# Kernel tuning notes

Hardware: AMD Instinct MI355X
Metric: run time of the kernel (lower is better)

The kernel has to match this reference:

```python
import jax, jax.numpy as jnp
import numpy as np


def setup_inputs() -> dict:
    key = jax.random.key(0)
    ks = jax.random.split(key, 9)
    B, S, I, H, L, O = 64, 1024, 64, 256, 2, 1
    sc = 1.0 / np.sqrt(H)
    return {
        "x": jax.random.normal(ks[0], (B, S, I), dtype=jnp.float32),
        "theta": jax.random.normal(ks[1], (I, H), dtype=jnp.float32) * 0.01,
        "phi": jax.random.normal(ks[2], (I, H), dtype=jnp.float32) * 0.01,
        "W_ih": jax.random.normal(ks[3], (L, 4 * H, H), dtype=jnp.float32) * sc,
        "W_hh": jax.random.normal(ks[4], (L, 4 * H, H), dtype=jnp.float32) * sc,
        "b_ih": jax.random.normal(ks[5], (L, 4 * H), dtype=jnp.float32) * sc,
        "b_hh": jax.random.normal(ks[6], (L, 4 * H), dtype=jnp.float32) * sc,
        "W_fc": jax.random.normal(ks[7], (O, H), dtype=jnp.float32) * sc,
        "b_fc": jax.random.normal(ks[8], (O,), dtype=jnp.float32) * sc,
    }


def _quantum(x, theta, phi):
    # Per-call Gaussian noise on the phase parameters (fixed key for determinism)
    k1, k2 = jax.random.split(jax.random.key(42))
    tn = jax.random.normal(k1, theta.shape, theta.dtype) * 0.01
    pn = jax.random.normal(k2, phi.shape, phi.dtype) * 0.01
    psi_r = jnp.cos(theta + tn)  # real part of psi
    psi_i = jnp.sin(phi + pn)    # imag part of psi
    # sum over input dim of x * psi == matmul; |complex| = sqrt(re^2 + im^2)
    yr = jnp.einsum('bsi,ih->bsh', x, psi_r)
    yi = jnp.einsum('bsi,ih->bsh', x, psi_i)
    return jnp.sqrt(yr * yr + yi * yi)


def _lstm_layer(inp, Wi, Wh, bi, bh):
    # inp: (B,S,H). PyTorch gate order: i, f, g, o.
    H = Wh.shape[-1]
    B = inp.shape[0]
    pre = jnp.einsum('bsh,gh->bsg', inp, Wi) + bi + bh  # (B,S,4H)

    def step(carry, xt):
        h, c = carry
        g = xt + h @ Wh.T
        i_, f_, g_, o_ = jnp.split(g, 4, axis=-1)
        i_ = jax.nn.sigmoid(i_)
        f_ = jax.nn.sigmoid(f_)
        o_ = jax.nn.sigmoid(o_)
        g_ = jnp.tanh(g_)
        c = f_ * c + i_ * g_
        h = o_ * jnp.tanh(c)
        return (h, c), h

    h0 = jnp.zeros((B, H), inp.dtype)
    (_, _), hs = jax.lax.scan(step, (h0, h0), jnp.swapaxes(pre, 0, 1))
    return jnp.swapaxes(hs, 0, 1)  # (B,S,H)


def reference(x, theta, phi, W_ih, W_hh, b_ih, b_hh, W_fc, b_fc):
    out = _quantum(x, theta, phi)
    for l in range(W_ih.shape[0]):
        out = _lstm_layer(out, W_ih[l], W_hh[l], b_ih[l], b_hh[l])
    return out[:, -1, :] @ W_fc.T + b_fc
```

## Files before the change

### kernel.cpp

```cpp
#include <hip/hip_runtime.h>

typedef _Float16 f16;
typedef _Float16 f16x2 __attribute__((ext_vector_type(2)));
typedef _Float16 f16x8 __attribute__((ext_vector_type(8)));
typedef float f32x4 __attribute__((ext_vector_type(4)));

#define B_ 64
#define S_ 1024
#define I_ 64
#define H_ 256
#define G_ 1024
#define M_ 65536

__device__ __forceinline__ unsigned rotl32(unsigned x, int r){ return (x<<r)|(x>>(32-r)); }

__device__ __forceinline__ void threefry(unsigned k0, unsigned k1, unsigned& x0, unsigned& x1){
  unsigned k2 = k0 ^ k1 ^ 0x1BD11BDAu;
  x0 += k0; x1 += k1;
  x0 += x1; x1 = rotl32(x1,13); x1 ^= x0;
  x0 += x1; x1 = rotl32(x1,15); x1 ^= x0;
  x0 += x1; x1 = rotl32(x1,26); x1 ^= x0;
  x0 += x1; x1 = rotl32(x1, 6); x1 ^= x0;
  x0 += k1; x1 += k2 + 1u;
  x0 += x1; x1 = rotl32(x1,17); x1 ^= x0;
  x0 += x1; x1 = rotl32(x1,29); x1 ^= x0;
  x0 += x1; x1 = rotl32(x1,16); x1 ^= x0;
  x0 += x1; x1 = rotl32(x1,24); x1 ^= x0;
  x0 += k2; x1 += k0 + 2u;
  x0 += x1; x1 = rotl32(x1,13); x1 ^= x0;
  x0 += x1; x1 = rotl32(x1,15); x1 ^= x0;
  x0 += x1; x1 = rotl32(x1,26); x1 ^= x0;
  x0 += x1; x1 = rotl32(x1, 6); x1 ^= x0;
  x0 += k0; x1 += k1 + 3u;
  x0 += x1; x1 = rotl32(x1,17); x1 ^= x0;
  x0 += x1; x1 = rotl32(x1,29); x1 ^= x0;
  x0 += x1; x1 = rotl32(x1,16); x1 ^= x0;
  x0 += x1; x1 = rotl32(x1,24); x1 ^= x0;
  x0 += k1; x1 += k2 + 4u;
  x0 += x1; x1 = rotl32(x1,13); x1 ^= x0;
  x0 += x1; x1 = rotl32(x1,15); x1 ^= x0;
  x0 += x1; x1 = rotl32(x1,26); x1 ^= x0;
  x0 += x1; x1 = rotl32(x1, 6); x1 ^= x0;
  x0 += k2; x1 += k0 + 5u;
}

__device__ __forceinline__ float erfinv_f(float x){
  float w = -log1pf(-x*x);
  float p;
  if (w < 5.f){
    w -= 2.5f;
    p = 2.81022636e-08f;
    p = fmaf(p,w, 3.43273939e-07f);
    p = fmaf(p,w,-3.5233877e-06f);
    p = fmaf(p,w,-4.39150654e-06f);
    p = fmaf(p,w, 0.00021858087f);
    p = fmaf(p,w,-0.00125372503f);
    p = fmaf(p,w,-0.00417768164f);
    p = fmaf(p,w, 0.246640727f);
    p = fmaf(p,w, 1.50140941f);
  } else {
    w = sqrtf(w) - 3.f;
    p = -0.000200214257f;
    p = fmaf(p,w, 0.000100950558f);
    p = fmaf(p,w, 0.00134934322f);
    p = fmaf(p,w,-0.00367342844f);
    p = fmaf(p,w, 0.00573950773f);
    p = fmaf(p,w,-0.0076224613f);
    p = fmaf(p,w, 0.00943887047f);
    p = fmaf(p,w, 1.00167406f);
    p = fmaf(p,w, 2.83297682f);
  }
  return p*x;
}

__device__ __forceinline__ float jax_normal_from_bits(unsigned bits){
  unsigned fb = (bits >> 9) | 0x3f800000u;
  float f = __uint_as_float(fb) - 1.0f;
  const float lo = -0.9999999403953552f;
  float u = fmaf(f, 2.0f, lo);
  u = fmaxf(lo, u);
  return 1.4142135623730951f * erfinv_f(u);
}

__global__ __launch_bounds__(256) void prep_psi(const float* __restrict__ theta,
                                                const float* __restrict__ phi,
                                                unsigned* __restrict__ psiP){
  int j = blockIdx.x*256 + threadIdx.x;
  unsigned a0=0u, a1=0u; threefry(0u,42u,a0,a1);
  unsigned b0=0u, b1=1u; threefry(0u,42u,b0,b1);
  unsigned t0=0u, t1=(unsigned)j; threefry(a0,a1,t0,t1);
  unsigned p0=0u, p1=(unsigned)j; threefry(b0,b1,p0,p1);
  float tn = 0.01f * jax_normal_from_bits(t0^t1);
  float pn = 0.01f * jax_normal_from_bits(p0^p1);
  float cr = cosf(theta[j] + tn);
  float ci = sinf(phi[j]   + pn);
  f16x2 pk; pk.x = (f16)cr; pk.y = (f16)ci;
  psiP[j] = __builtin_bit_cast(unsigned, pk);
}

__global__ __launch_bounds__(256) void pack_wh(const float* __restrict__ Whh,
                                               uint4* __restrict__ WhT4){
  int idx = blockIdx.x*256 + threadIdx.x;
  int l   = idx >> 15;
  int row = (idx >> 5) & 1023;
  int kk  = idx & 31;
  const float* src = Whh + ((size_t)(l*1024 + row))*256 + kk*8;
  f16x8 tmp;
  #pragma unroll
  for (int j=0;j<8;j++) tmp[j] = (f16)src[j];
  WhT4[l*32768 + kk*1024 + row] = __builtin_bit_cast(uint4, tmp);
}

__global__ __launch_bounds__(256) void pack_wi_bias(const float* __restrict__ Wih,
                                                    const float* __restrict__ bih,
                                                    const float* __restrict__ bhh,
                                                    f16* __restrict__ WiH,
                                                    float* __restrict__ biasS){
  int idx = blockIdx.x*256 + threadIdx.x;
  WiH[idx] = (f16)Wih[idx];
  if (idx < 2048) biasS[idx] = bih[idx] + bhh[idx];
}

__global__ __launch_bounds__(128) void zero_prog(int* __restrict__ p){
  p[threadIdx.x] = 0;
}

__global__ __launch_bounds__(256) void quantum_k(const float* __restrict__ x,
                                                 const unsigned* __restrict__ psiP,
                                                 f16* __restrict__ yq){
  __shared__ float xs[64];
  int m = blockIdx.x;
  int n = threadIdx.x;
  if (n < 64) xs[n] = x[(size_t)m*64 + n];
  __syncthreads();
  float ar=0.f, ai=0.f;
  #pragma unroll 8
  for (int k=0;k<64;k++){
    unsigned p = psiP[k*256 + n];
    f16x2 pk = __builtin_bit_cast(f16x2, p);
    float xv = xs[k];
    ar = fmaf(xv, (float)pk.x, ar);
    ai = fmaf(xv, (float)pk.y, ai);
  }
  yq[(size_t)m*256 + n] = (f16)sqrtf(ar*ar + ai*ai);
}

__global__ __launch_bounds__(256,2) void pre_gemm(const f16* __restrict__ A,
                                                  const f16* __restrict__ W,
                                                  const float* __restrict__ bias,
                                                  f16* __restrict__ out){
  const int m0 = blockIdx.x*64;
  const int n0 = blockIdx.y*512;
  __shared__ f16 As[64*264];
  const int tid = threadIdx.x;
  #pragma unroll
  for (int it=0; it<8; ++it){
    int u = tid + it*256;
    int row = u >> 5, ko = u & 31;
    f16x8 v = *(const f16x8*)(A + (size_t)(m0+row)*256 + ko*8);
    *(f16x8*)(&As[row*264 + ko*8]) = v;
  }
  __syncthreads();
  const int wave = tid >> 6, lane = tid & 63;
  const int n_w = n0 + wave*128;
  const int lr = lane & 15, lk = (lane>>4)*8;
  f32x4 acc[4][8] = {};
  for (int ks=0; ks<8; ++ks){
    f16x8 a[4];
    #pragma unroll
    for (int mt=0; mt<4; ++mt)
      a[mt] = *(const f16x8*)(&As[(mt*16+lr)*264 + ks*32 + lk]);
    #pragma unroll
    for (int nt=0; nt<8; ++nt){
      f16x8 b = *(const f16x8*)(W + (size_t)(n_w + nt*16 + lr)*256 + ks*32 + lk);
      #pragma unroll
      for (int mt=0; mt<4; ++mt)
        acc[mt][nt] = __builtin_amdgcn_mfma_f32_16x16x32_f16(a[mt], b, acc[mt][nt], 0,0,0);
    }
  }
  const int col = lr, rbase = (lane>>4)*4;
  #pragma unroll
  for (int nt=0; nt<8; ++nt){
    float bv = bias[n_w + nt*16 + col];
    #pragma unroll
    for (int mt=0; mt<4; ++mt){
      #pragma unroll
      for (int j=0; j<4; ++j){
        int m = m0 + mt*16 + rbase + j;
        out[(size_t)m*1024 + n_w + nt*16 + col] = (f16)(acc[mt][nt][j] + bv);
      }
    }
  }
}

__device__ __forceinline__ float sigm_f(float x){
  x = fminf(fmaxf(x,-30.f),30.f);
  return 1.f/(1.f + __expf(-x));
}
__device__ __forceinline__ float tanh_f(float x){
  x = fminf(fmaxf(x,-15.f),15.f);
  float e = __expf(-2.f*x);
  return (1.f-e)/(1.f+e);
}
__device__ __forceinline__ float dot2f(unsigned w, unsigned h, float acc){
#if __has_builtin(__builtin_amdgcn_fdot2)
  return __builtin_amdgcn_fdot2(__builtin_bit_cast(f16x2,w), __builtin_bit_cast(f16x2,h), acc, false);
#else
  float d;
  asm("v_dot2_f32_f16 %0, %1, %2, %3" : "=v"(d) : "v"(w), "v"(h), "v"(acc));
  return d;
#endif
}

__device__ __forceinline__ f32x4 mfma16(uint4 a, uint4 b, f32x4 c){
  return __builtin_amdgcn_mfma_f32_16x16x32_f16(
      __builtin_bit_cast(f16x8, a), __builtin_bit_cast(f16x8, b), c, 0, 0, 0);
}

template<int WRITE_ALL, int CONSUME>
__device__ __forceinline__
void lstm_core(const f16* __restrict__ preB,
               const uint4* __restrict__ Wh,
               f16* __restrict__ outh,
               f16* __restrict__ hfin_p,
               int* __restrict__ prog_rel,
               int* __restrict__ prog_acq,
               uint4* wlds, uint4* h4, float* gbuf)
{
  const int tid = threadIdx.x;
  uint4 w[23];
  #pragma unroll
  for (int j=0;j<23;++j) w[j] = Wh[j*1024 + tid];
  #pragma unroll
  for (int j=0;j<5;++j)  wlds[j*1024 + tid] = Wh[(23+j)*1024 + tid];
  if (tid < 32) h4[tid] = make_uint4(0u,0u,0u,0u);
  float c = 0.f;

  if (CONSUME){
    if (tid==0){
      while (__hip_atomic_load(prog_acq, __ATOMIC_ACQUIRE, __HIP_MEMORY_SCOPE_AGENT) < 1)
        __builtin_amdgcn_s_sleep(8);
    }
  }
  __syncthreads();

  float pv = (float)preB[tid];
  const int gtype = tid >> 8;
  const uint4* wstr = Wh + 28*1024 + tid;

  for (int t=0; t<1024; ++t){
    if (CONSUME){
      if ((t&15)==15 && t<1023){
        if (tid==0){
          const int need = ((t+1)>>4) + 1;
          while (__hip_atomic_load(prog_acq, __ATOMIC_ACQUIRE, __HIP_MEMORY_SCOPE_AGENT) < need)
            __builtin_amdgcn_s_sleep(8);
        }
        __syncthreads();
      }
    }
    float pn = (t < 1023) ? (float)preB[(size_t)(t+1)*1024 + tid] : 0.f;
    uint4 s0 = wstr[0];
    uint4 s1 = wstr[1024];
    uint4 s2 = wstr[2048];
    uint4 s3 = wstr[3072];
    float a0 = pv, a1 = 0.f;

    uint4 hb0 = h4[0], hb1 = h4[1];
    uint4 ub0 = wlds[tid], ub1 = wlds[1024 + tid];

    #pragma unroll
    for (int kk=0; kk<23; ++kk){
      uint4 hp = (kk & 1) ? hb1 : hb0;
      if (kk & 1) hb1 = h4[kk+2]; else hb0 = h4[kk+2];
      a0 = dot2f(w[kk].x, hp.x, a0); a1 = dot2f(w[kk].y, hp.y, a1);
      a0 = dot2f(w[kk].z, hp.z, a0); a1 = dot2f(w[kk].w, hp.w, a1);
    }
    #pragma unroll
    for (int j=0; j<5; ++j){
      const int kk = 23 + j;
      uint4 hp = (kk & 1) ? hb1 : hb0;
      if (kk & 1) hb1 = h4[kk+2]; else hb0 = h4[kk+2];
      uint4 u = (j & 1) ? ub1 : ub0;
      if (j + 2 < 5){ if (j & 1) ub1 = wlds[(j+2)*1024 + tid]; else ub0 = wlds[(j+2)*1024 + tid]; }
      a0 = dot2f(u.x, hp.x, a0); a1 = dot2f(u.y, hp.y, a1);
      a0 = dot2f(u.z, hp.z, a0); a1 = dot2f(u.w, hp.w, a1);
    }
    #pragma unroll
    for (int j=0; j<4; ++j){
      const int kk = 28 + j;
      uint4 hp = (kk & 1) ? hb1 : hb0;
      if (kk + 2 < 32){ if (kk & 1) hb1 = h4[kk+2]; else hb0 = h4[kk+2]; }
      const uint4 u = (j==0) ? s0 : (j==1) ? s1 : (j==2) ? s2 : s3;
      a0 = dot2f(u.x, hp.x, a0); a1 = dot2f(u.y, hp.y, a1);
      a0 = dot2f(u.z, hp.z, a0); a1 = dot2f(u.w, hp.w, a1);
    }

    {
      const float raw = a0 + a1;
      gbuf[tid] = (gtype == 2) ? tanh_f(raw) : sigm_f(raw);
    }
    __syncthreads();
    if (tid < 256){
      float i_ = gbuf[tid];
      float f_ = gbuf[256+tid];
      float g_ = gbuf[512+tid];
      float o_ = gbuf[768+tid];
      c = fmaf(f_, c, i_*g_);
      float h = o_ * tanh_f(c);
      ((f16*)h4)[tid] = (f16)h;
      if (WRITE_ALL) outh[(size_t)t*256 + tid] = (f16)h;
      else if (t == 1023) hfin_p[tid] = (f16)h;
    }
    __syncthreads();
    if (WRITE_ALL){
      if ((t&15)==15 && tid==0){
        __threadfence();
        __hip_atomic_store(prog_rel, t+1, __ATOMIC_RELEASE, __HIP_MEMORY_SCOPE_AGENT);
      }
    }
    pv = pn;
  }
}

__device__ __forceinline__
void gemm_role(const f16* __restrict__ h1b,
               const f16* __restrict__ W2,
               const float* __restrict__ bias2,
               f16* __restrict__ pre2b,
               int* __restrict__ prog1b,
               int* __restrict__ prog2b)
{
  const int tid  = threadIdx.x;
  const int w    = tid >> 6, lane = tid & 63;
  const int lr   = lane & 15, lq = lane >> 4;
  for (int cidx=0; cidx<64; ++cidx){
    if (tid==0){
      while (__hip_atomic_load(prog1b, __ATOMIC_ACQUIRE, __HIP_MEMORY_SCOPE_AGENT) < 16*(cidx+1))
        __builtin_amdgcn_s_sleep(8);
    }
    __syncthreads();
    const int t0 = cidx*16;
    const f16* Ab = h1b + ((size_t)(t0 + lr))*256 + lq*8;
    uint4 af[8];
    #pragma unroll
    for (int ks=0; ks<8; ++ks) af[ks] = *(const uint4*)(Ab + ks*32);
    #pragma unroll
    for (int nt=0; nt<4; ++nt){
      f32x4 acc = {0.f,0.f,0.f,0.f};
      const int gate = w*64 + nt*16 + lr;
      const f16* Bb = W2 + (size_t)gate*256 + lq*8;
      #pragma unroll
      for (int ks=0; ks<8; ++ks){
        const uint4 bf = *(const uint4*)(Bb + ks*32);
        acc = mfma16(af[ks], bf, acc);
      }
      const float bv = bias2[gate];
      #pragma unroll
      for (int j=0; j<4; ++j){
        const int t = t0 + lq*4 + j;
        pre2b[(size_t)t*1024 + gate] = (f16)(acc[j] + bv);
      }
    }
    asm volatile("s_waitcnt vmcnt(0)" ::: "memory");
    __syncthreads();
    if (tid==0){
      __threadfence();
      __hip_atomic_store(prog2b, cidx+1, __ATOMIC_RELEASE, __HIP_MEMORY_SCOPE_AGENT);
    }
  }
}

__global__ __launch_bounds__(1024, 4)
void pipeline_k(const f16* __restrict__ pre1,
                const uint4* __restrict__ WhT4,
                const f16* __restrict__ W2,
                const float* __restrict__ biasS,
                f16* __restrict__ h1,
                f16* __restrict__ pre2,
                f16* __restrict__ hfin,
                int* __restrict__ prog1,
                int* __restrict__ prog2)
{
  __shared__ __align__(16) uint4 wlds[5*1024];
  __shared__ __align__(16) uint4 h4[32];
  __shared__ float gbuf[1024];
  const int bid = blockIdx.x;
  if (bid < 64){
    const int b = bid;
    lstm_core<1,0>(pre1 + (size_t)b*1024*1024, WhT4,
                   h1 + (size_t)b*1024*256, nullptr,
                   prog1 + b, nullptr, wlds, h4, gbuf);
  } else if (bid < 128){
    const int b = bid - 64;
    gemm_role(h1 + (size_t)b*1024*256, W2, biasS + 1024,
              pre2 + (size_t)b*1024*1024, prog1 + b, prog2 + b);
  } else {
    const int b = bid - 128;
    lstm_core<0,1>(pre2 + (size_t)b*1024*1024, WhT4 + 32768,
                   nullptr, hfin + b*256,
                   nullptr, prog2 + b, wlds, h4, gbuf);
  }
}

__global__ __launch_bounds__(64) void fc_k(const f16* __restrict__ hfin,
                                           const float* __restrict__ Wfc,
                                           const float* __restrict__ bfc,
                                           float* __restrict__ out){
  int b = blockIdx.x, k = threadIdx.x;
  float a = 0.f;
  #pragma unroll
  for (int j=0;j<4;j++){
    int idx = k + 64*j;
    a += (float)hfin[b*256 + idx] * Wfc[idx];
  }
  #pragma unroll
  for (int off=32; off; off>>=1) a += __shfl_down(a, off);
  if (k==0) out[b] = a + bfc[0];
}

extern "C" void kernel_launch(void* const* d_in, const int* in_sizes, int n_in,
                              void* d_out, int out_size, void* d_ws, size_t ws_size,
                              hipStream_t stream) {
  const float* x     = (const float*)d_in[0];
  const float* theta = (const float*)d_in[1];
  const float* phi   = (const float*)d_in[2];
  const float* Wih   = (const float*)d_in[3];
  const float* Whh   = (const float*)d_in[4];
  const float* bih   = (const float*)d_in[5];
  const float* bhh   = (const float*)d_in[6];
  const float* Wfc   = (const float*)d_in[7];
  const float* bfc   = (const float*)d_in[8];
  float* out = (float*)d_out;

  char* ws = (char*)d_ws;
  size_t off = 0;
  auto take = [&](size_t bytes){ size_t r = off; off += (bytes + 255) & ~(size_t)255; return r; };
  f16*      pre1  = (f16*)     (ws + take((size_t)M_*1024*2));
  f16*      pre2  = pre1;
  f16*      yq    = (f16*)     (ws + take((size_t)M_*256*2));
  f16*      h1    = (f16*)     (ws + take((size_t)M_*256*2));
  unsigned* psiP  = (unsigned*)(ws + take((size_t)16384*4));
  uint4*    WhT4  = (uint4*)   (ws + take((size_t)2*32768*16));
  f16*      WiH   = (f16*)     (ws + take((size_t)2*262144*2));
  float*    biasS = (float*)   (ws + take((size_t)2048*4));
  f16*      hfin  = (f16*)     (ws + take((size_t)64*256*2));
  int*      prog1 = (int*)     (ws + take((size_t)64*4));
  int*      prog2 = (int*)     (ws + take((size_t)64*4));

  zero_prog   <<<1,    128, 0, stream>>>(prog1);
  prep_psi    <<<64,   256, 0, stream>>>(theta, phi, psiP);
  pack_wh     <<<256,  256, 0, stream>>>(Whh, WhT4);
  pack_wi_bias<<<2048, 256, 0, stream>>>(Wih, bih, bhh, WiH, biasS);
  quantum_k   <<<65536,256, 0, stream>>>(x, psiP, yq);

  dim3 gg(1024, 2);
  pre_gemm <<<gg, 256, 0, stream>>>(yq, WiH, biasS, pre1);

  pipeline_k <<<192, 1024, 0, stream>>>(pre1, WhT4, WiH + 262144, biasS,
                                        h1, pre2, hfin, prog1, prog2);

  fc_k <<<64, 64, 0, stream>>>(hfin, Wfc, bfc, out);
}
```

Before: 2.604 ms.

## Remap gate rows so LSTM gate combine uses wave shuffles and double-buffered h

Permutes the gate-row assignment so each group of four adjacent lanes holds the i, f, g and o gates for one hidden unit. The gates are then combined with in-wave shuffles instead of a shared-memory gate buffer. The hidden state is double-buffered in LDS, which removes one of the two per-timestep block barriers on the serial recurrence. The trade-off is that only a quarter of the threads do the cell update, and the weight and pre-activation loads use a strided remapped index.

```diff
diff --git a/kernel.cpp b/kernel.cpp
--- a/kernel.cpp
+++ b/kernel.cpp
@@ -225,15 +225,21 @@
                f16* __restrict__ hfin_p,
                int* __restrict__ prog_rel,
                int* __restrict__ prog_acq,
-               uint4* wlds, uint4* h4, float* gbuf)
+               uint4* wlds, uint4* h4)
 {
-  const int tid = threadIdx.x;
+  const int tid  = threadIdx.x;
+  const int rmp  = (tid & 3)*256 + (tid >> 2);
+  const int lane = tid & 63;
+  const int qb   = lane & ~3;
+  const int gt   = tid & 3;
+  const int e    = tid >> 2;
+
   uint4 w[23];
   #pragma unroll
-  for (int j=0;j<23;++j) w[j] = Wh[j*1024 + tid];
-  #pragma unroll
-  for (int j=0;j<5;++j)  wlds[j*1024 + tid] = Wh[(23+j)*1024 + tid];
-  if (tid < 32) h4[tid] = make_uint4(0u,0u,0u,0u);
+  for (int j=0;j<23;++j) w[j] = Wh[j*1024 + rmp];
+  #pragma unroll
+  for (int j=0;j<5;++j)  wlds[j*1024 + tid] = Wh[(23+j)*1024 + rmp];
+  if (tid < 64) h4[tid] = make_uint4(0u,0u,0u,0u);
   float c = 0.f;
 
   if (CONSUME){
@@ -244,9 +250,8 @@
   }
   __syncthreads();
 
-  float pv = (float)preB[tid];
-  const int gtype = tid >> 8;
-  const uint4* wstr = Wh + 28*1024 + tid;
+  float pv = (float)preB[rmp];
+  const uint4* wstr = Wh + 28*1024 + rmp;
 
   for (int t=0; t<1024; ++t){
     if (CONSUME){
@@ -259,20 +264,21 @@
         __syncthreads();
       }
     }
-    float pn = (t < 1023) ? (float)preB[(size_t)(t+1)*1024 + tid] : 0.f;
+    float pn = (t < 1023) ? (float)preB[(size_t)(t+1)*1024 + rmp] : 0.f;
     uint4 s0 = wstr[0];
     uint4 s1 = wstr[1024];
     uint4 s2 = wstr[2048];
     uint4 s3 = wstr[3072];
     float a0 = pv, a1 = 0.f;
 
-    uint4 hb0 = h4[0], hb1 = h4[1];
+    const uint4* hr = h4 + (t&1)*32;
+    uint4 hb0 = hr[0], hb1 = hr[1];
     uint4 ub0 = wlds[tid], ub1 = wlds[1024 + tid];
 
     #pragma unroll
     for (int kk=0; kk<23; ++kk){
       uint4 hp = (kk & 1) ? hb1 : hb0;
-      if (kk & 1) hb1 = h4[kk+2]; else hb0 = h4[kk+2];
+      if (kk & 1) hb1 = hr[kk+2]; else hb0 = hr[kk+2];
       a0 = dot2f(w[kk].x, hp.x, a0); a1 = dot2f(w[kk].y, hp.y, a1);
       a0 = dot2f(w[kk].z, hp.z, a0); a1 = dot2f(w[kk].w, hp.w, a1);
     }
@@ -280,7 +286,7 @@
     for (int j=0; j<5; ++j){
       const int kk = 23 + j;
       uint4 hp = (kk & 1) ? hb1 : hb0;
-      if (kk & 1) hb1 = h4[kk+2]; else hb0 = h4[kk+2];
+      if (kk & 1) hb1 = hr[kk+2]; else hb0 = hr[kk+2];
       uint4 u = (j & 1) ? ub1 : ub0;
       if (j + 2 < 5){ if (j & 1) ub1 = wlds[(j+2)*1024 + tid]; else ub0 = wlds[(j+2)*1024 + tid]; }
       a0 = dot2f(u.x, hp.x, a0); a1 = dot2f(u.y, hp.y, a1);
@@ -290,27 +296,27 @@
     for (int j=0; j<4; ++j){
       const int kk = 28 + j;
       uint4 hp = (kk & 1) ? hb1 : hb0;
-      if (kk + 2 < 32){ if (kk & 1) hb1 = h4[kk+2]; else hb0 = h4[kk+2]; }
+      if (kk + 2 < 32){ if (kk & 1) hb1 = hr[kk+2]; else hb0 = hr[kk+2]; }
       const uint4 u = (j==0) ? s0 : (j==1) ? s1 : (j==2) ? s2 : s3;
       a0 = dot2f(u.x, hp.x, a0); a1 = dot2f(u.y, hp.y, a1);
       a0 = dot2f(u.z, hp.z, a0); a1 = dot2f(u.w, hp.w, a1);
     }
 
-    {
-      const float raw = a0 + a1;
-      gbuf[tid] = (gtype == 2) ? tanh_f(raw) : sigm_f(raw);
-    }
-    __syncthreads();
-    if (tid < 256){
-      float i_ = gbuf[tid];
-      float f_ = gbuf[256+tid];
-      float g_ = gbuf[512+tid];
-      float o_ = gbuf[768+tid];
-      c = fmaf(f_, c, i_*g_);
-      float h = o_ * tanh_f(c);
-      ((f16*)h4)[tid] = (f16)h;
-      if (WRITE_ALL) outh[(size_t)t*256 + tid] = (f16)h;
-      else if (t == 1023) hfin_p[tid] = (f16)h;
+    const float raw = a0 + a1;
+    const float act = (gt == 2) ? tanh_f(raw) : sigm_f(raw);
+
+    const float iv = __shfl(act, qb + 0, 64);
+    const float fv = __shfl(act, qb + 1, 64);
+    const float gv = __shfl(act, qb + 2, 64);
+    const float ov = __shfl(act, qb + 3, 64);
+
+    if (gt == 0){
+      c = fmaf(fv, c, iv*gv);
+      const float h = ov * tanh_f(c);
+      const f16 hf = (f16)h;
+      ((f16*)(h4 + ((t+1)&1)*32))[e] = hf;
+      if (WRITE_ALL) outh[(size_t)t*256 + e] = hf;
+      else if (t == 1023) hfin_p[e] = hf;
     }
     __syncthreads();
     if (WRITE_ALL){
@@ -383,14 +389,13 @@
                 int* __restrict__ prog2)
 {
   __shared__ __align__(16) uint4 wlds[5*1024];
-  __shared__ __align__(16) uint4 h4[32];
-  __shared__ float gbuf[1024];
+  __shared__ __align__(16) uint4 h4[64];
   const int bid = blockIdx.x;
   if (bid < 64){
     const int b = bid;
     lstm_core<1,0>(pre1 + (size_t)b*1024*1024, WhT4,
                    h1 + (size_t)b*1024*256, nullptr,
-                   prog1 + b, nullptr, wlds, h4, gbuf);
+                   prog1 + b, nullptr, wlds, h4);
   } else if (bid < 128){
     const int b = bid - 64;
     gemm_role(h1 + (size_t)b*1024*256, W2, biasS + 1024,
@@ -399,7 +404,7 @@
     const int b = bid - 128;
     lstm_core<0,1>(pre2 + (size_t)b*1024*1024, WhT4 + 32768,
                    nullptr, hfin + b*256,
-                   nullptr, prog2 + b, wlds, h4, gbuf);
+                   nullptr, prog2 + b, wlds, h4);
   }
 }
 
```

Measured after the change: 2.780 ms. 1.07x slower.
